# Performance work log

Hardware: AMD Instinct MI355X
Metric: run time of the kernel (lower is better)

## Reference

```python
import jax, jax.numpy as jnp
import numpy as np

V, E, HT, HC = 30000, 300, 256, 256
B, LC, T = 32, 32, 64
NTAG = 9  # output_dim + 2


def lstm_dir(x, lens, Wih, Whh, b, reverse):
    """Variable-length single-direction LSTM (packed-sequence semantics).
    x: [N, T, D], lens: [N] int. Returns outputs [N, T, H] zeroed at pad steps.
    Masked state update keeps h,c frozen at pad steps, so reverse=True starts
    from each sequence's true last element (zeros carry through leading pads).
    """
    N, Tn, _ = x.shape
    H = Whh.shape[1]
    gx = jnp.einsum('ntd,gd->ntg', x, Wih) + b            # [N,T,4H]
    mask = jnp.arange(Tn)[None, :] < lens[:, None]         # [N,T]

    def step(carry, inp):
        h, c = carry
        g_t, m = inp                                       # [N,4H], [N]
        gates = g_t + h @ Whh.T
        i, f, g, o = jnp.split(gates, 4, axis=-1)
        c_new = jax.nn.sigmoid(f) * c + jax.nn.sigmoid(i) * jnp.tanh(g)
        h_new = jax.nn.sigmoid(o) * jnp.tanh(c_new)
        m = m[:, None]
        h2 = jnp.where(m, h_new, h)
        c2 = jnp.where(m, c_new, c)
        return (h2, c2), jnp.where(m, h2, 0.0)

    init = (jnp.zeros((N, H), x.dtype), jnp.zeros((N, H), x.dtype))
    xs = (jnp.swapaxes(gx, 0, 1), mask.T)
    _, ys = jax.lax.scan(step, init, xs, reverse=reverse)
    return jnp.swapaxes(ys, 0, 1)                          # [N,T,H]


def bilstm(x, lens, Wih_f, Whh_f, b_f, Wih_b, Whh_b, b_b):
    hf = lstm_dir(x, lens, Wih_f, Whh_f, b_f, reverse=False)
    hb = lstm_dir(x, lens, Wih_b, Whh_b, b_b, reverse=True)
    return jnp.concatenate([hf, hb], axis=-1)


def setup_inputs() -> dict:
    key = jax.random.key(0)
    ks = jax.random.split(key, 20)
    s = 0.05
    inp = {
        'x': jax.random.randint(ks[0], (B, LC, T), 0, V, dtype=jnp.int32),
        'x_feats': jax.random.normal(ks[1], (B, LC, 64), jnp.float32),
        'x_len': jnp.maximum(jax.random.randint(ks[2], (B,), 0, LC, dtype=jnp.int32), 1),
        'x_chunk_len': jax.random.randint(ks[3], (B, LC), 1, T + 1, dtype=jnp.int32),
        'emb': jax.random.normal(ks[4], (V, E), jnp.float32) * s,
        'tok_Wih_f': jax.random.normal(ks[5], (4 * HT, E), jnp.float32) * s,
        'tok_Whh_f': jax.random.normal(ks[6], (4 * HT, HT), jnp.float32) * s,
        'tok_b_f': jax.random.normal(ks[7], (4 * HT,), jnp.float32) * s,
        'tok_Wih_b': jax.random.normal(ks[8], (4 * HT, E), jnp.float32) * s,
        'tok_Whh_b': jax.random.normal(ks[9], (4 * HT, HT), jnp.float32) * s,
        'tok_b_b': jax.random.normal(ks[10], (4 * HT,), jnp.float32) * s,
        'chk_Wih_f': jax.random.normal(ks[11], (4 * HC, 2 * HT), jnp.float32) * s,
        'chk_Whh_f': jax.random.normal(ks[12], (4 * HC, HC), jnp.float32) * s,
        'chk_b_f': jax.random.normal(ks[13], (4 * HC,), jnp.float32) * s,
        'chk_Wih_b': jax.random.normal(ks[14], (4 * HC, 2 * HT), jnp.float32) * s,
        'chk_Whh_b': jax.random.normal(ks[15], (4 * HC, HC), jnp.float32) * s,
        'chk_b_b': jax.random.normal(ks[16], (4 * HC,), jnp.float32) * s,
        'fc_W': jax.random.normal(ks[17], (NTAG, 2 * HC), jnp.float32) * s,
        'fc_b': jax.random.normal(ks[18], (NTAG,), jnp.float32) * s,
    }
    return inp


def reference(x, x_feats, x_len, x_chunk_len, emb,
              tok_Wih_f, tok_Whh_f, tok_b_f, tok_Wih_b, tok_Whh_b, tok_b_b,
              chk_Wih_f, chk_Whh_f, chk_b_f, chk_Wih_b, chk_Whh_b, chk_b_b,
              fc_W, fc_b):
    b, lc, t = x.shape
    xe = emb[x].reshape(b * lc, t, -1)                     # [B*LC, T, E]
    clens = jnp.clip(x_chunk_len.reshape(-1), 1, t)        # [B*LC]
    h = bilstm(xe, clens, tok_Wih_f, tok_Whh_f, tok_b_f,
               tok_Wih_b, tok_Whh_b, tok_b_b)              # [B*LC, T, 2HT]
    # gather output at last valid timestep (= [fwd final, bwd one-step])
    last = h[jnp.arange(b * lc), clens - 1]                # [B*LC, 2HT]
    chunks = last.reshape(b, lc, -1)                       # [B, LC, 2HT]
    ch = bilstm(chunks, x_len, chk_Wih_f, chk_Whh_f, chk_b_f,
                chk_Wih_b, chk_Whh_b, chk_b_b)             # [B, LC, 2HC]
    # pad_packed(total_length=LC) gives zeros at pad -> fc sees zeros there
    out = ch @ fc_W.T + fc_b                               # [B, LC, NTAG]
    return out
```

## Files before the change

kernel.cpp:

```cpp
#include <hip/hip_runtime.h>


typedef __attribute__((ext_vector_type(8))) short s16x8;
typedef __attribute__((ext_vector_type(4))) float f32x4;
typedef __attribute__((ext_vector_type(2))) unsigned int u32x2;

__device__ __forceinline__ unsigned short f2bf(float f) {
  unsigned u = __builtin_bit_cast(unsigned, f);
  u += 0x7fff + ((u >> 16) & 1);
  return (unsigned short)(u >> 16);
}
__device__ __forceinline__ float bf2f(unsigned short h) {
  unsigned u = ((unsigned)h) << 16;
  return __builtin_bit_cast(float, u);
}
__device__ __forceinline__ float sigm(float x) { return 1.f / (1.f + __expf(-x)); }
__device__ __forceinline__ float tanh_(float x) { return 1.f - 2.f / (__expf(2.f * x) + 1.f); }

union PK8 { s16x8 v; unsigned short u[8]; };

__global__ void prep_weights(const float* __restrict__ wihf, const float* __restrict__ wihb,
                             const float* __restrict__ wcf, const float* __restrict__ wcb,
                             unsigned short* __restrict__ o_wf, unsigned short* __restrict__ o_wb,
                             unsigned short* __restrict__ o_wcf, unsigned short* __restrict__ o_wcb) {
  const int job = blockIdx.y, r = blockIdx.x, tid = threadIdx.x;
  const float* src; unsigned short* dst; int Ks, Kd;
  switch (job) {
    case 0: src = wihf; dst = o_wf;   Ks = 300; Kd = 320; break;
    case 1: src = wihb; dst = o_wb;   Ks = 300; Kd = 320; break;
    case 2: src = wcf;  dst = o_wcf;  Ks = 512; Kd = 512; break;
    default:src = wcb;  dst = o_wcb;  Ks = 512; Kd = 512; break;
  }
  for (int c = tid; c < Kd; c += 256)
    dst[r * Kd + c] = f2bf(c < Ks ? src[r * Ks + c] : 0.f);
}

__global__ __launch_bounds__(256)
void prep_whh_frag(const float* __restrict__ w0, const float* __restrict__ w1,
                   const float* __restrict__ w2,
                   unsigned short* __restrict__ o0, unsigned short* __restrict__ o1,
                   unsigned short* __restrict__ o2) {
  const float* src = blockIdx.y == 0 ? w0 : (blockIdx.y == 1 ? w1 : w2);
  unsigned short* dst = blockIdx.y == 0 ? o0 : (blockIdx.y == 1 ? o1 : o2);
  const int fid = blockIdx.x;
  const int b = fid & 1, g = (fid >> 1) & 3, kt = (fid >> 3) & 7, js = fid >> 6;
  for (int i = threadIdx.x; i < 512; i += 256) {
    const int lane = i >> 3, e = i & 7;
    const int cc = lane & 15, qq = lane >> 4;
    const int row = g * 256 + (js * 2 + b) * 16 + cc;
    const int col = kt * 32 + qq * 8 + e;
    dst[(size_t)fid * 512 + i] = f2bf(src[row * 256 + col]);
  }
}

__global__ void prep_small(const int* __restrict__ x, const int* __restrict__ xcl,
                           int* __restrict__ clens, int* __restrict__ lastv,
                           int* __restrict__ order, int* __restrict__ glen) {
  __shared__ int start[65];
  const int n = threadIdx.x;
  if (n < 65) start[n] = 0;
  __syncthreads();
  int len = xcl[n]; len = len < 1 ? 1 : (len > 64 ? 64 : len);
  clens[n] = len;
  lastv[n] = x[n * 64 + len - 1];
  atomicAdd(&start[len], 1);
  __syncthreads();
  if (n == 0) {
    int acc = 0;
    for (int l = 64; l >= 1; --l) { int h = start[l]; start[l] = acc; acc += h; }
  }
  __syncthreads();
  int pos = atomicAdd(&start[len], 1);
  order[pos] = n;
  __syncthreads();
  if (n < 64) glen[n] = clens[order[n * 16]];
}

__global__ __launch_bounds__(256, 2)
void gemm_bf(const float* __restrict__ A, const int* __restrict__ rowmap,
             int Mrows, int Astride, int Klog, int KP,
             const unsigned short* __restrict__ B, unsigned short* __restrict__ C) {
  __shared__ unsigned short As[128 * 40];
  __shared__ unsigned short Ep[4][64 * 136];
  const int tid = threadIdx.x;
  const int lane = tid & 63, w = tid >> 6;
  const int wrow = w >> 1, wcol = w & 1;
  const int cc = lane & 15, qq = lane >> 4;
  const int m0 = blockIdx.y * 128, n0 = blockIdx.x * 256;

  f32x4 zz = {0.f, 0.f, 0.f, 0.f};
  f32x4 acc[4][8];
#pragma unroll
  for (int i = 0; i < 4; ++i)
#pragma unroll
    for (int j = 0; j < 8; ++j) acc[i][j] = zz;

  const int arow = tid >> 1, ahalf = tid & 1;
  const float* arp = nullptr;
  {
    int av = m0 + arow;
    if (av < Mrows) {
      int amap = rowmap ? rowmap[av] : av;
      arp = A + (long)amap * Astride;
    }
  }

  const int nktiles = KP >> 5;
  for (int kt = 0; kt < nktiles; ++kt) {
    const int k0 = kt << 5;
    __syncthreads();
    {
      const int kb = k0 + ahalf * 16;
      unsigned short hv[16];
      if (arp && kb + 16 <= Klog) {
        const float* p = arp + kb;
#pragma unroll
        for (int i = 0; i < 16; i += 4) {
          f32x4 t = *(const f32x4*)(p + i);
          hv[i] = f2bf(t.x); hv[i + 1] = f2bf(t.y);
          hv[i + 2] = f2bf(t.z); hv[i + 3] = f2bf(t.w);
        }
      } else {
#pragma unroll
        for (int i = 0; i < 16; ++i) {
          float v = (arp && (kb + i) < Klog) ? arp[kb + i] : 0.f;
          hv[i] = f2bf(v);
        }
      }
      PK8 p0, p1;
#pragma unroll
      for (int i = 0; i < 8; ++i) { p0.u[i] = hv[i]; p1.u[i] = hv[8 + i]; }
      *(s16x8*)&As[arow * 40 + ahalf * 16] = p0.v;
      *(s16x8*)&As[arow * 40 + ahalf * 16 + 8] = p1.v;
    }
    __syncthreads();
    s16x8 af[4];
#pragma unroll
    for (int mt = 0; mt < 4; ++mt)
      af[mt] = *(const s16x8*)&As[(wrow * 64 + mt * 16 + cc) * 40 + qq * 8];
#pragma unroll
    for (int nt = 0; nt < 8; ++nt) {
      const unsigned short* bp = B + (long)(n0 + wcol * 128 + nt * 16 + cc) * KP + k0 + qq * 8;
      s16x8 bfr = *(const s16x8*)bp;
#pragma unroll
      for (int mt = 0; mt < 4; ++mt)
        acc[mt][nt] = __builtin_amdgcn_mfma_f32_16x16x32_bf16(af[mt], bfr, acc[mt][nt], 0, 0, 0);
    }
  }
  __syncthreads();
#pragma unroll
  for (int mt = 0; mt < 4; ++mt)
#pragma unroll
    for (int nt = 0; nt < 8; ++nt)
#pragma unroll
      for (int r = 0; r < 4; ++r)
        Ep[w][(mt * 16 + qq * 4 + r) * 136 + nt * 16 + cc] = f2bf(acc[mt][nt][r]);
  __syncthreads();
#pragma unroll
  for (int it = 0; it < 16; ++it) {
    int row = it * 4 + qq;
    s16x8 d = *(const s16x8*)&Ep[w][row * 136 + cc * 8];
    int gm = m0 + wrow * 64 + row;
    int gn = n0 + wcol * 128 + cc * 8;
    if (gm < Mrows) *(s16x8*)&C[(long)gm * 1024 + gn] = d;
  }
}

__global__ void bwd_step(const unsigned short* __restrict__ gxb,
                         const float* __restrict__ bias,
                         float* __restrict__ chunks) {
  const int n = blockIdx.x, j = threadIdx.x;
  const unsigned short* row = gxb + (long)n * 1024;
  float gi = bf2f(row[j]) + bias[j];
  float gg = bf2f(row[512 + j]) + bias[512 + j];
  float go = bf2f(row[768 + j]) + bias[768 + j];
  float cn = sigm(gi) * tanh_(gg);
  chunks[(long)n * 512 + 256 + j] = sigm(go) * tanh_(cn);
}

__global__ __launch_bounds__(256)
void gather_gx(const unsigned short* __restrict__ proj, const int* __restrict__ x,
               const int* __restrict__ order, const int* __restrict__ clens,
               const int* __restrict__ glen, const float* __restrict__ bias,
               unsigned short* __restrict__ gx) {
  const int t = blockIdx.x, p = blockIdx.y, j = threadIdx.x;
  if (t >= glen[p >> 4]) return;
  const int seq = order[p];
  const int len = clens[seq];
  if (t >= len) return;
  unsigned short* dst = gx + (((size_t)(p >> 4) * 64 + t) * 16 + (p & 15)) * 1024 + j * 4;
  const int tok = x[seq * 64 + t];
  const unsigned short* src = proj + (size_t)tok * 1024 + j;
  unsigned v0 = f2bf(bf2f(src[0]) + bias[j]);
  unsigned v1 = f2bf(bf2f(src[256]) + bias[256 + j]);
  unsigned v2 = f2bf(bf2f(src[512]) + bias[512 + j]);
  unsigned v3 = f2bf(bf2f(src[768]) + bias[768 + j]);
  u32x2 pk = {v0 | (v1 << 16), v2 | (v3 << 16)};
  *(u32x2*)dst = pk;
}

__global__ __launch_bounds__(256)
void repack4(const unsigned short* __restrict__ s0, const unsigned short* __restrict__ s1,
             const float* __restrict__ b0, const float* __restrict__ b1,
             unsigned short* __restrict__ d0, unsigned short* __restrict__ d1) {
  const int r = blockIdx.x, j = threadIdx.x;
  const int m = r >> 5, t = r & 31;
  const int mg = m >> 4, m16 = m & 15;
  const unsigned short* s = (blockIdx.y ? s1 : s0) + (size_t)r * 1024;
  const float* bb = blockIdx.y ? b1 : b0;
  unsigned short* d = (blockIdx.y ? d1 : d0) +
                      (size_t)((mg * 32 + t) * 16 + m16) * 1024 + j * 4;
  unsigned v0 = f2bf(bf2f(s[j]) + bb[j]);
  unsigned v1 = f2bf(bf2f(s[256 + j]) + bb[256 + j]);
  unsigned v2 = f2bf(bf2f(s[512 + j]) + bb[512 + j]);
  unsigned v3 = f2bf(bf2f(s[768 + j]) + bb[768 + j]);
  u32x2 pk = {v0 | (v1 << 16), v2 | (v3 << 16)};
  *(u32x2*)d = pk;
}

__global__ __launch_bounds__(1024, 4)
void tok_fwd(const unsigned short* __restrict__ gx,
             const unsigned short* __restrict__ WhP,
             const int* __restrict__ order,
             const int* __restrict__ clens,
             const int* __restrict__ glen,
             float* __restrict__ chunks) {
  extern __shared__ unsigned short smem[];
  unsigned short* hbuf = smem;
  unsigned short* ldsW = smem + 8448;
  int* sg = (int*)(smem + 8448 + 65536);
  int* slen = sg + 16;

  const int tid = threadIdx.x;
  const int lane = tid & 63, w = tid >> 6;
  const int cc = lane & 15, qq = lane >> 4;
  const int gb = blockIdx.x;

  if (tid < 16) {
    int s = order[gb * 16 + tid];
    sg[tid] = s;
    slen[tid] = clens[s];
  }
  for (int i = tid; i < 4224; i += 1024) hbuf[i] = 0;

  const unsigned short* wgl = WhP + ((size_t)(w >> 1) * 64 + (w & 1)) * 512 + lane * 8;
  {
    unsigned short* ld = ldsW + w * 4096 + lane * 8;
#pragma unroll
    for (int kt = 0; kt < 2; ++kt)
#pragma unroll
      for (int g = 0; g < 4; ++g)
        *(s16x8*)&ld[(kt * 4 + g) * 512] = *(const s16x8*)&wgl[(kt * 8 + g * 2) * 512];
  }
  s16x8 Rw[24];
#pragma unroll
  for (int kt = 2; kt < 8; ++kt)
#pragma unroll
    for (int g = 0; g < 4; ++g)
      Rw[(kt - 2) * 4 + g] = *(const s16x8*)&wgl[(kt * 8 + g * 2) * 512];

  __syncthreads();

  const int maxlen = glen[gb];
  const int j = w * 16 + cc;
  int lenr[4];
#pragma unroll
  for (int r = 0; r < 4; ++r) lenr[r] = slen[qq * 4 + r];

  float cst[4];
  unsigned short hreg[4];
#pragma unroll
  for (int r = 0; r < 4; ++r) { cst[r] = 0.f; hreg[r] = 0; }

  const unsigned short* gx0 = gx + (size_t)gb * 64 * 16 * 1024 + j * 4;
  const unsigned short* ldw = ldsW + w * 4096 + lane * 8;
  f32x4 zz = {0.f, 0.f, 0.f, 0.f};

  for (int t = 0; t < maxlen; ++t) {
    const unsigned short* hr = hbuf + (t & 1) * 4224;
    unsigned short* hw = hbuf + ((t & 1) ^ 1) * 4224;

    __syncthreads();

    u32x2 gxp[4];
#pragma unroll
    for (int r = 0; r < 4; ++r)
      gxp[r] = *(const u32x2*)(gx0 + ((size_t)t * 16 + qq * 4 + r) * 1024);

    f32x4 acc[4];
#pragma unroll
    for (int g = 0; g < 4; ++g) acc[g] = zz;

#pragma unroll
    for (int kt = 0; kt < 2; ++kt) {
      s16x8 a0 = *(const s16x8*)&hr[cc * 264 + kt * 32 + qq * 8];
#pragma unroll
      for (int g = 0; g < 4; ++g) {
        s16x8 bf = *(const s16x8*)&ldw[(kt * 4 + g) * 512];
        acc[g] = __builtin_amdgcn_mfma_f32_16x16x32_bf16(a0, bf, acc[g], 0, 0, 0);
      }
    }
#pragma unroll
    for (int kt = 2; kt < 8; ++kt) {
      s16x8 a0 = *(const s16x8*)&hr[cc * 264 + kt * 32 + qq * 8];
#pragma unroll
      for (int g = 0; g < 4; ++g)
        acc[g] = __builtin_amdgcn_mfma_f32_16x16x32_bf16(a0, Rw[(kt - 2) * 4 + g], acc[g], 0, 0, 0);
    }

#pragma unroll
    for (int r = 0; r < 4; ++r) {
      const int m = qq * 4 + r;
      const u32x2 pk = gxp[r];
      float gi = acc[0][r] + bf2f((unsigned short)(pk.x & 0xffff));
      float gf = acc[1][r] + bf2f((unsigned short)(pk.x >> 16));
      float gg = acc[2][r] + bf2f((unsigned short)(pk.y & 0xffff));
      float go = acc[3][r] + bf2f((unsigned short)(pk.y >> 16));
      if (t < lenr[r]) {
        float cn = sigm(gf) * cst[r] + sigm(gi) * tanh_(gg);
        cst[r] = cn;
        hreg[r] = f2bf(sigm(go) * tanh_(cn));
      }
      hw[m * 264 + j] = hreg[r];
    }
  }

#pragma unroll
  for (int r = 0; r < 4; ++r)
    chunks[(size_t)sg[qq * 4 + r] * 512 + j] = bf2f(hreg[r]);
}

__global__ __launch_bounds__(1024, 4)
void chunk_rec(const unsigned short* __restrict__ gxf,
               const unsigned short* __restrict__ gxb,
               const unsigned short* __restrict__ WhPf,
               const unsigned short* __restrict__ WhPb,
               const int* __restrict__ xlen,
               unsigned short* __restrict__ ch) {
  extern __shared__ unsigned short smem[];
  unsigned short* hbuf = smem;
  unsigned short* ldsW = smem + 8448;

  const int tid = threadIdx.x;
  const int lane = tid & 63, w = tid >> 6;
  const int cc = lane & 15, qq = lane >> 4;
  const int dir = blockIdx.x & 1, mg = blockIdx.x >> 1;
  const unsigned short* gx = (dir ? gxb : gxf) + (size_t)mg * 32 * 16 * 1024;
  const unsigned short* WhP = dir ? WhPb : WhPf;

  for (int i = tid; i < 4224; i += 1024) hbuf[i] = 0;

  const unsigned short* wgl = WhP + ((size_t)(w >> 1) * 64 + (w & 1)) * 512 + lane * 8;
  {
    unsigned short* ld = ldsW + w * 4096 + lane * 8;
#pragma unroll
    for (int kt = 0; kt < 2; ++kt)
#pragma unroll
      for (int g = 0; g < 4; ++g)
        *(s16x8*)&ld[(kt * 4 + g) * 512] = *(const s16x8*)&wgl[(kt * 8 + g * 2) * 512];
  }
  s16x8 Rw[24];
#pragma unroll
  for (int kt = 2; kt < 8; ++kt)
#pragma unroll
    for (int g = 0; g < 4; ++g)
      Rw[(kt - 2) * 4 + g] = *(const s16x8*)&wgl[(kt * 8 + g * 2) * 512];

  __syncthreads();

  const int j = w * 16 + cc;
  int lenr[4];
#pragma unroll
  for (int r = 0; r < 4; ++r) {
    int L = xlen[mg * 16 + qq * 4 + r];
    lenr[r] = L > 32 ? 32 : L;
  }

  float cst[4];
  unsigned short hreg[4];
#pragma unroll
  for (int r = 0; r < 4; ++r) { cst[r] = 0.f; hreg[r] = 0; }

  const unsigned short* ldw = ldsW + w * 4096 + lane * 8;
  f32x4 zz = {0.f, 0.f, 0.f, 0.f};

  for (int tt = 0; tt < 32; ++tt) {
    const int t = dir ? (31 - tt) : tt;
    const unsigned short* hr = hbuf + (tt & 1) * 4224;
    unsigned short* hw = hbuf + ((tt & 1) ^ 1) * 4224;

    __syncthreads();

    u32x2 gxp[4];
#pragma unroll
    for (int r = 0; r < 4; ++r)
      gxp[r] = *(const u32x2*)(gx + ((size_t)t * 16 + qq * 4 + r) * 1024 + j * 4);

    f32x4 acc[4];
#pragma unroll
    for (int g = 0; g < 4; ++g) acc[g] = zz;

#pragma unroll
    for (int kt = 0; kt < 2; ++kt) {
      s16x8 a0 = *(const s16x8*)&hr[cc * 264 + kt * 32 + qq * 8];
#pragma unroll
      for (int g = 0; g < 4; ++g) {
        s16x8 bf = *(const s16x8*)&ldw[(kt * 4 + g) * 512];
        acc[g] = __builtin_amdgcn_mfma_f32_16x16x32_bf16(a0, bf, acc[g], 0, 0, 0);
      }
    }
#pragma unroll
    for (int kt = 2; kt < 8; ++kt) {
      s16x8 a0 = *(const s16x8*)&hr[cc * 264 + kt * 32 + qq * 8];
#pragma unroll
      for (int g = 0; g < 4; ++g)
        acc[g] = __builtin_amdgcn_mfma_f32_16x16x32_bf16(a0, Rw[(kt - 2) * 4 + g], acc[g], 0, 0, 0);
    }

#pragma unroll
    for (int r = 0; r < 4; ++r) {
      const int m = qq * 4 + r;
      const u32x2 pk = gxp[r];
      float gi = acc[0][r] + bf2f((unsigned short)(pk.x & 0xffff));
      float gf = acc[1][r] + bf2f((unsigned short)(pk.x >> 16));
      float gg = acc[2][r] + bf2f((unsigned short)(pk.y & 0xffff));
      float go = acc[3][r] + bf2f((unsigned short)(pk.y >> 16));
      unsigned short out16 = 0;
      if (t < lenr[r]) {
        float cn = sigm(gf) * cst[r] + sigm(gi) * tanh_(gg);
        cst[r] = cn;
        hreg[r] = f2bf(sigm(go) * tanh_(cn));
        out16 = hreg[r];
      }
      hw[m * 264 + j] = hreg[r];
      ch[(size_t)((mg * 16 + m) * 32 + t) * 512 + dir * 256 + j] = out16;
    }
  }
}

__global__ __launch_bounds__(64)
void fc_kernel(const unsigned short* __restrict__ ch, const float* __restrict__ W,
               const float* __restrict__ bfc, float* __restrict__ out) {
  const int n = blockIdx.x, lane = threadIdx.x;
  float xv[8];
  const unsigned short* cp = ch + (long)n * 512 + lane * 8;
#pragma unroll
  for (int i = 0; i < 8; ++i) xv[i] = bf2f(cp[i]);
  float s[9];
#pragma unroll
  for (int k = 0; k < 9; ++k) {
    const float* wr = W + k * 512 + lane * 8;
    float t = 0.f;
#pragma unroll
    for (int i = 0; i < 8; ++i) t += xv[i] * wr[i];
    s[k] = t;
  }
#pragma unroll
  for (int off = 32; off; off >>= 1)
#pragma unroll
    for (int k = 0; k < 9; ++k) s[k] += __shfl_down(s[k], off, 64);
  if (lane == 0) {
#pragma unroll
    for (int k = 0; k < 9; ++k) out[n * 9 + k] = s[k] + bfc[k];
  }
}

extern "C" void kernel_launch(void* const* d_in, const int* in_sizes, int n_in,
                              void* d_out, int out_size, void* d_ws, size_t ws_size,
                              hipStream_t stream) {
  const int*   x           = (const int*)d_in[0];
  const int*   x_len       = (const int*)d_in[2];
  const int*   x_chunk_len = (const int*)d_in[3];
  const float* emb         = (const float*)d_in[4];
  const float* tok_Wih_f   = (const float*)d_in[5];
  const float* tok_Whh_f   = (const float*)d_in[6];
  const float* tok_b_f     = (const float*)d_in[7];
  const float* tok_Wih_b   = (const float*)d_in[8];
  const float* tok_b_b     = (const float*)d_in[10];
  const float* chk_Wih_f   = (const float*)d_in[11];
  const float* chk_Whh_f   = (const float*)d_in[12];
  const float* chk_b_f     = (const float*)d_in[13];
  const float* chk_Wih_b   = (const float*)d_in[14];
  const float* chk_Whh_b   = (const float*)d_in[15];
  const float* chk_b_b     = (const float*)d_in[16];
  const float* fc_W        = (const float*)d_in[17];
  const float* fc_b        = (const float*)d_in[18];
  float* out = (float*)d_out;

  char* ws = (char*)d_ws;
  size_t off = 0;
  auto alloc = [&](size_t bytes) -> void* {
    void* p = ws + off;
    off += (bytes + 255) & ~(size_t)255;
    return p;
  };
  unsigned short* Wf   = (unsigned short*)alloc((size_t)1024 * 320 * 2);
  unsigned short* Wb   = (unsigned short*)alloc((size_t)1024 * 320 * 2);
  unsigned short* Wcf  = (unsigned short*)alloc((size_t)1024 * 512 * 2);
  unsigned short* Wcb  = (unsigned short*)alloc((size_t)1024 * 512 * 2);
  unsigned short* WhPtok=(unsigned short*)alloc((size_t)512 * 512 * 2);
  unsigned short* WhPcf= (unsigned short*)alloc((size_t)512 * 512 * 2);
  unsigned short* WhPcb= (unsigned short*)alloc((size_t)512 * 512 * 2);
  unsigned short* proj = (unsigned short*)alloc((size_t)30000 * 1024 * 2);
  unsigned short* gxbb = (unsigned short*)alloc((size_t)1024 * 1024 * 2);
  unsigned short* gxcf = (unsigned short*)alloc((size_t)1024 * 1024 * 2);
  unsigned short* gxcb = (unsigned short*)alloc((size_t)1024 * 1024 * 2);
  unsigned short* gxcfp= (unsigned short*)alloc((size_t)1024 * 1024 * 2);
  unsigned short* gxcbp= (unsigned short*)alloc((size_t)1024 * 1024 * 2);
  float*          chunks = (float*)alloc((size_t)1024 * 512 * 4);
  unsigned short* cho  = (unsigned short*)alloc((size_t)1024 * 512 * 2);
  unsigned short* gxs  = (unsigned short*)alloc((size_t)1024 * 64 * 1024 * 2);
  int* clens = (int*)alloc(1024 * 4);
  int* lastv = (int*)alloc(1024 * 4);
  int* order = (int*)alloc(1024 * 4);
  int* glen  = (int*)alloc(64 * 4);

  hipFuncSetAttribute((const void*)tok_fwd,
                      hipFuncAttributeMaxDynamicSharedMemorySize, 148096);
  hipFuncSetAttribute((const void*)chunk_rec,
                      hipFuncAttributeMaxDynamicSharedMemorySize, 147968);

  prep_weights<<<dim3(1024, 4), 256, 0, stream>>>(
      tok_Wih_f, tok_Wih_b, chk_Wih_f, chk_Wih_b, Wf, Wb, Wcf, Wcb);
  prep_whh_frag<<<dim3(512, 3), 256, 0, stream>>>(
      tok_Whh_f, chk_Whh_f, chk_Whh_b, WhPtok, WhPcf, WhPcb);
  prep_small<<<1, 1024, 0, stream>>>(x, x_chunk_len, clens, lastv, order, glen);

  gemm_bf<<<dim3(4, 235), 256, 0, stream>>>(emb, nullptr, 30000, 300, 300, 320, Wf, proj);
  gemm_bf<<<dim3(4, 8), 256, 0, stream>>>(emb, lastv, 1024, 300, 300, 320, Wb, gxbb);
  bwd_step<<<1024, 256, 0, stream>>>(gxbb, tok_b_b, chunks);
  gather_gx<<<dim3(64, 1024), 256, 0, stream>>>(proj, x, order, clens, glen, tok_b_f, gxs);
  tok_fwd<<<64, 1024, 148096, stream>>>(gxs, WhPtok, order, clens, glen, chunks);
  gemm_bf<<<dim3(4, 8), 256, 0, stream>>>(chunks, nullptr, 1024, 512, 512, 512, Wcf, gxcf);
  gemm_bf<<<dim3(4, 8), 256, 0, stream>>>(chunks, nullptr, 1024, 512, 512, 512, Wcb, gxcb);
  repack4<<<dim3(1024, 2), 256, 0, stream>>>(gxcf, gxcb, chk_b_f, chk_b_b, gxcfp, gxcbp);
  chunk_rec<<<4, 1024, 147968, stream>>>(gxcfp, gxcbp, WhPcf, WhPcb, x_len, cho);
  fc_kernel<<<1024, 64, 0, stream>>>(cho, fc_W, fc_b, out);
}
```

Baseline: 883.6 us.

## Stream recurrent weights from global each step instead of pinning in registers

The recurrent Whh fragments are reordered so each wave's 32 fragments are contiguous. Only the first 8 stay in LDS; the remaining 24 are reloaded from global/L2 every timestep, double-buffered through S/T register sets and overlapped with the MFMAs. This frees the 24 s16x8 registers that used to hold weights, which should lower register pressure and spilling, at the cost of per-step global weight traffic on the serial critical path. The hbuf zeroing now clears both double buffers.

```diff
diff --git a/kernel.cpp b/kernel.cpp
--- a/kernel.cpp
+++ b/kernel.cpp
@@ -4,6 +4,7 @@
 typedef __attribute__((ext_vector_type(8))) short s16x8;
 typedef __attribute__((ext_vector_type(4))) float f32x4;
 typedef __attribute__((ext_vector_type(2))) unsigned int u32x2;
+typedef __attribute__((ext_vector_type(4))) unsigned int u32x4;
 
 __device__ __forceinline__ unsigned short f2bf(float f) {
   unsigned u = __builtin_bit_cast(unsigned, f);
@@ -43,11 +44,11 @@
   const float* src = blockIdx.y == 0 ? w0 : (blockIdx.y == 1 ? w1 : w2);
   unsigned short* dst = blockIdx.y == 0 ? o0 : (blockIdx.y == 1 ? o1 : o2);
   const int fid = blockIdx.x;
-  const int b = fid & 1, g = (fid >> 1) & 3, kt = (fid >> 3) & 7, js = fid >> 6;
+  const int g = fid & 3, kt = (fid >> 2) & 7, jt = fid >> 5;
   for (int i = threadIdx.x; i < 512; i += 256) {
     const int lane = i >> 3, e = i & 7;
     const int cc = lane & 15, qq = lane >> 4;
-    const int row = g * 256 + (js * 2 + b) * 16 + cc;
+    const int row = g * 256 + jt * 16 + cc;
     const int col = kt * 32 + qq * 8 + e;
     dst[(size_t)fid * 512 + i] = f2bf(src[row * 256 + col]);
   }
@@ -241,28 +242,18 @@
     sg[tid] = s;
     slen[tid] = clens[s];
   }
-  for (int i = tid; i < 4224; i += 1024) hbuf[i] = 0;
-
-  const unsigned short* wgl = WhP + ((size_t)(w >> 1) * 64 + (w & 1)) * 512 + lane * 8;
+  for (int i = tid; i < 8448; i += 1024) hbuf[i] = 0;
+
+  const unsigned short* wgl = WhP + ((size_t)w * 8 * 4) * 512 + lane * 8;
   {
     unsigned short* ld = ldsW + w * 4096 + lane * 8;
 #pragma unroll
-    for (int kt = 0; kt < 2; ++kt)
-#pragma unroll
-      for (int g = 0; g < 4; ++g)
-        *(s16x8*)&ld[(kt * 4 + g) * 512] = *(const s16x8*)&wgl[(kt * 8 + g * 2) * 512];
-  }
-  s16x8 Rw[24];
-#pragma unroll
-  for (int kt = 2; kt < 8; ++kt)
-#pragma unroll
-    for (int g = 0; g < 4; ++g)
-      Rw[(kt - 2) * 4 + g] = *(const s16x8*)&wgl[(kt * 8 + g * 2) * 512];
-
+    for (int s = 0; s < 8; ++s)
+      *(s16x8*)&ld[s * 512] = *(const s16x8*)&wgl[s * 512];
+  }
   __syncthreads();
 
   const int maxlen = glen[gb];
-  const int j = w * 16 + cc;
   int lenr[4];
 #pragma unroll
   for (int r = 0; r < 4; ++r) lenr[r] = slen[qq * 4 + r];
@@ -270,8 +261,9 @@
   float cst[4];
   unsigned short hreg[4];
 #pragma unroll
-  for (int r = 0; r < 4; ++r) { cst[r] = 0.f; hreg[r] = 0; }
-
+  for (int i = 0; i < 4; ++i) { cst[i] = 0.f; hreg[i] = 0; }
+
+  const int j = w * 16 + cc;
   const unsigned short* gx0 = gx + (size_t)gb * 64 * 16 * 1024 + j * 4;
   const unsigned short* ldw = ldsW + w * 4096 + lane * 8;
   f32x4 zz = {0.f, 0.f, 0.f, 0.f};
@@ -282,30 +274,77 @@
 
     __syncthreads();
 
+    s16x8 S[4], T[4];
+#pragma unroll
+    for (int g4 = 0; g4 < 4; ++g4)
+      S[g4] = *(const s16x8*)&wgl[(8 + g4) * 512];
     u32x2 gxp[4];
 #pragma unroll
     for (int r = 0; r < 4; ++r)
       gxp[r] = *(const u32x2*)(gx0 + ((size_t)t * 16 + qq * 4 + r) * 1024);
+#pragma unroll
+    for (int g4 = 0; g4 < 4; ++g4)
+      T[g4] = *(const s16x8*)&wgl[(12 + g4) * 512];
 
     f32x4 acc[4];
 #pragma unroll
-    for (int g = 0; g < 4; ++g) acc[g] = zz;
+    for (int g4 = 0; g4 < 4; ++g4) acc[g4] = zz;
 
 #pragma unroll
     for (int kt = 0; kt < 2; ++kt) {
-      s16x8 a0 = *(const s16x8*)&hr[cc * 264 + kt * 32 + qq * 8];
-#pragma unroll
-      for (int g = 0; g < 4; ++g) {
-        s16x8 bf = *(const s16x8*)&ldw[(kt * 4 + g) * 512];
-        acc[g] = __builtin_amdgcn_mfma_f32_16x16x32_bf16(a0, bf, acc[g], 0, 0, 0);
-      }
-    }
-#pragma unroll
-    for (int kt = 2; kt < 8; ++kt) {
-      s16x8 a0 = *(const s16x8*)&hr[cc * 264 + kt * 32 + qq * 8];
-#pragma unroll
-      for (int g = 0; g < 4; ++g)
-        acc[g] = __builtin_amdgcn_mfma_f32_16x16x32_bf16(a0, Rw[(kt - 2) * 4 + g], acc[g], 0, 0, 0);
+      s16x8 a = *(const s16x8*)&hr[cc * 264 + kt * 32 + qq * 8];
+#pragma unroll
+      for (int g4 = 0; g4 < 4; ++g4)
+        acc[g4] = __builtin_amdgcn_mfma_f32_16x16x32_bf16(
+            a, *(const s16x8*)&ldw[(kt * 4 + g4) * 512], acc[g4], 0, 0, 0);
+    }
+    {
+      s16x8 a = *(const s16x8*)&hr[cc * 264 + 2 * 32 + qq * 8];
+#pragma unroll
+      for (int g4 = 0; g4 < 4; ++g4)
+        acc[g4] = __builtin_amdgcn_mfma_f32_16x16x32_bf16(a, S[g4], acc[g4], 0, 0, 0);
+    }
+#pragma unroll
+    for (int g4 = 0; g4 < 4; ++g4)
+      S[g4] = *(const s16x8*)&wgl[(16 + g4) * 512];
+    {
+      s16x8 a = *(const s16x8*)&hr[cc * 264 + 3 * 32 + qq * 8];
+#pragma unroll
+      for (int g4 = 0; g4 < 4; ++g4)
+        acc[g4] = __builtin_amdgcn_mfma_f32_16x16x32_bf16(a, T[g4], acc[g4], 0, 0, 0);
+    }
+#pragma unroll
+    for (int g4 = 0; g4 < 4; ++g4)
+      T[g4] = *(const s16x8*)&wgl[(20 + g4) * 512];
+    {
+      s16x8 a = *(const s16x8*)&hr[cc * 264 + 4 * 32 + qq * 8];
+#pragma unroll
+      for (int g4 = 0; g4 < 4; ++g4)
+        acc[g4] = __builtin_amdgcn_mfma_f32_16x16x32_bf16(a, S[g4], acc[g4], 0, 0, 0);
+    }
+#pragma unroll
+    for (int g4 = 0; g4 < 4; ++g4)
+      S[g4] = *(const s16x8*)&wgl[(24 + g4) * 512];
+    {
+      s16x8 a = *(const s16x8*)&hr[cc * 264 + 5 * 32 + qq * 8];
+#pragma unroll
+      for (int g4 = 0; g4 < 4; ++g4)
+        acc[g4] = __builtin_amdgcn_mfma_f32_16x16x32_bf16(a, T[g4], acc[g4], 0, 0, 0);
+    }
+#pragma unroll
+    for (int g4 = 0; g4 < 4; ++g4)
+      T[g4] = *(const s16x8*)&wgl[(28 + g4) * 512];
+    {
+      s16x8 a = *(const s16x8*)&hr[cc * 264 + 6 * 32 + qq * 8];
+#pragma unroll
+      for (int g4 = 0; g4 < 4; ++g4)
+        acc[g4] = __builtin_amdgcn_mfma_f32_16x16x32_bf16(a, S[g4], acc[g4], 0, 0, 0);
+    }
+    {
+      s16x8 a = *(const s16x8*)&hr[cc * 264 + 7 * 32 + qq * 8];
+#pragma unroll
+      for (int g4 = 0; g4 < 4; ++g4)
+        acc[g4] = __builtin_amdgcn_mfma_f32_16x16x32_bf16(a, T[g4], acc[g4], 0, 0, 0);
     }
 
 #pragma unroll
@@ -348,24 +387,15 @@
   const unsigned short* gx = (dir ? gxb : gxf) + (size_t)mg * 32 * 16 * 1024;
   const unsigned short* WhP = dir ? WhPb : WhPf;
 
-  for (int i = tid; i < 4224; i += 1024) hbuf[i] = 0;
-
-  const unsigned short* wgl = WhP + ((size_t)(w >> 1) * 64 + (w & 1)) * 512 + lane * 8;
+  for (int i = tid; i < 8448; i += 1024) hbuf[i] = 0;
+
+  const unsigned short* wgl = WhP + ((size_t)w * 8 * 4) * 512 + lane * 8;
   {
     unsigned short* ld = ldsW + w * 4096 + lane * 8;
 #pragma unroll
-    for (int kt = 0; kt < 2; ++kt)
-#pragma unroll
-      for (int g = 0; g < 4; ++g)
-        *(s16x8*)&ld[(kt * 4 + g) * 512] = *(const s16x8*)&wgl[(kt * 8 + g * 2) * 512];
-  }
-  s16x8 Rw[24];
-#pragma unroll
-  for (int kt = 2; kt < 8; ++kt)
-#pragma unroll
-    for (int g = 0; g < 4; ++g)
-      Rw[(kt - 2) * 4 + g] = *(const s16x8*)&wgl[(kt * 8 + g * 2) * 512];
-
+    for (int s = 0; s < 8; ++s)
+      *(s16x8*)&ld[s * 512] = *(const s16x8*)&wgl[s * 512];
+  }
   __syncthreads();
 
   const int j = w * 16 + cc;
@@ -379,7 +409,7 @@
   float cst[4];
   unsigned short hreg[4];
 #pragma unroll
-  for (int r = 0; r < 4; ++r) { cst[r] = 0.f; hreg[r] = 0; }
+  for (int i = 0; i < 4; ++i) { cst[i] = 0.f; hreg[i] = 0; }
 
   const unsigned short* ldw = ldsW + w * 4096 + lane * 8;
   f32x4 zz = {0.f, 0.f, 0.f, 0.f};
@@ -391,30 +421,77 @@
 
     __syncthreads();
 
+    s16x8 S[4], T[4];
+#pragma unroll
+    for (int g4 = 0; g4 < 4; ++g4)
+      S[g4] = *(const s16x8*)&wgl[(8 + g4) * 512];
     u32x2 gxp[4];
 #pragma unroll
     for (int r = 0; r < 4; ++r)
       gxp[r] = *(const u32x2*)(gx + ((size_t)t * 16 + qq * 4 + r) * 1024 + j * 4);
+#pragma unroll
+    for (int g4 = 0; g4 < 4; ++g4)
+      T[g4] = *(const s16x8*)&wgl[(12 + g4) * 512];
 
     f32x4 acc[4];
 #pragma unroll
-    for (int g = 0; g < 4; ++g) acc[g] = zz;
+    for (int g4 = 0; g4 < 4; ++g4) acc[g4] = zz;
 
 #pragma unroll
     for (int kt = 0; kt < 2; ++kt) {
-      s16x8 a0 = *(const s16x8*)&hr[cc * 264 + kt * 32 + qq * 8];
-#pragma unroll
-      for (int g = 0; g < 4; ++g) {
-        s16x8 bf = *(const s16x8*)&ldw[(kt * 4 + g) * 512];
-        acc[g] = __builtin_amdgcn_mfma_f32_16x16x32_bf16(a0, bf, acc[g], 0, 0, 0);
-      }
-    }
-#pragma unroll
-    for (int kt = 2; kt < 8; ++kt) {
-      s16x8 a0 = *(const s16x8*)&hr[cc * 264 + kt * 32 + qq * 8];
-#pragma unroll
-      for (int g = 0; g < 4; ++g)
-        acc[g] = __builtin_amdgcn_mfma_f32_16x16x32_bf16(a0, Rw[(kt - 2) * 4 + g], acc[g], 0, 0, 0);
+      s16x8 a = *(const s16x8*)&hr[cc * 264 + kt * 32 + qq * 8];
+#pragma unroll
+      for (int g4 = 0; g4 < 4; ++g4)
+        acc[g4] = __builtin_amdgcn_mfma_f32_16x16x32_bf16(
+            a, *(const s16x8*)&ldw[(kt * 4 + g4) * 512], acc[g4], 0, 0, 0);
+    }
+    {
+      s16x8 a = *(const s16x8*)&hr[cc * 264 + 2 * 32 + qq * 8];
+#pragma unroll
+      for (int g4 = 0; g4 < 4; ++g4)
+        acc[g4] = __builtin_amdgcn_mfma_f32_16x16x32_bf16(a, S[g4], acc[g4], 0, 0, 0);
+    }
+#pragma unroll
+    for (int g4 = 0; g4 < 4; ++g4)
+      S[g4] = *(const s16x8*)&wgl[(16 + g4) * 512];
+    {
+      s16x8 a = *(const s16x8*)&hr[cc * 264 + 3 * 32 + qq * 8];
+#pragma unroll
+      for (int g4 = 0; g4 < 4; ++g4)
+        acc[g4] = __builtin_amdgcn_mfma_f32_16x16x32_bf16(a, T[g4], acc[g4], 0, 0, 0);
+    }
+#pragma unroll
+    for (int g4 = 0; g4 < 4; ++g4)
+      T[g4] = *(const s16x8*)&wgl[(20 + g4) * 512];
+    {
+      s16x8 a = *(const s16x8*)&hr[cc * 264 + 4 * 32 + qq * 8];
+#pragma unroll
+      for (int g4 = 0; g4 < 4; ++g4)
+        acc[g4] = __builtin_amdgcn_mfma_f32_16x16x32_bf16(a, S[g4], acc[g4], 0, 0, 0);
+    }
+#pragma unroll
+    for (int g4 = 0; g4 < 4; ++g4)
+      S[g4] = *(const s16x8*)&wgl[(24 + g4) * 512];
+    {
+      s16x8 a = *(const s16x8*)&hr[cc * 264 + 5 * 32 + qq * 8];
+#pragma unroll
+      for (int g4 = 0; g4 < 4; ++g4)
+        acc[g4] = __builtin_amdgcn_mfma_f32_16x16x32_bf16(a, T[g4], acc[g4], 0, 0, 0);
+    }
+#pragma unroll
+    for (int g4 = 0; g4 < 4; ++g4)
+      T[g4] = *(const s16x8*)&wgl[(28 + g4) * 512];
+    {
+      s16x8 a = *(const s16x8*)&hr[cc * 264 + 6 * 32 + qq * 8];
+#pragma unroll
+      for (int g4 = 0; g4 < 4; ++g4)
+        acc[g4] = __builtin_amdgcn_mfma_f32_16x16x32_bf16(a, S[g4], acc[g4], 0, 0, 0);
+    }
+    {
+      s16x8 a = *(const s16x8*)&hr[cc * 264 + 7 * 32 + qq * 8];
+#pragma unroll
+      for (int g4 = 0; g4 < 4; ++g4)
+        acc[g4] = __builtin_amdgcn_mfma_f32_16x16x32_bf16(a, T[g4], acc[g4], 0, 0, 0);
     }
 
 #pragma unroll
```

Result: slower. 933.4 us (+5.6%).

## Stream recurrent weights per step via double-buffered global-to-LDS loads

Applied to the files above, without the earlier changes.

Both recurrent kernels stop keeping the Whh fragments resident in LDS plus registers. Each timestep they now stream the fragments from global memory into two per-wave LDS stage buffers with global_load_lds, interleaving the loads with the MFMAs using explicit vmcnt and lgkmcnt waits. The weight fragment layout in prep_whh_frag is reordered so each wave reads one contiguous block. This removes about 96 VGPRs of register-held weights, but every step now re-reads the whole weight matrix from L2, which adds memory traffic and wait latency to the serial recurrence.

```diff
diff --git a/kernel.cpp b/kernel.cpp
--- a/kernel.cpp
+++ b/kernel.cpp
@@ -4,6 +4,7 @@
 typedef __attribute__((ext_vector_type(8))) short s16x8;
 typedef __attribute__((ext_vector_type(4))) float f32x4;
 typedef __attribute__((ext_vector_type(2))) unsigned int u32x2;
+typedef __attribute__((ext_vector_type(4))) unsigned int u32x4;
 
 __device__ __forceinline__ unsigned short f2bf(float f) {
   unsigned u = __builtin_bit_cast(unsigned, f);
@@ -16,6 +17,27 @@
 }
 __device__ __forceinline__ float sigm(float x) { return 1.f / (1.f + __expf(-x)); }
 __device__ __forceinline__ float tanh_(float x) { return 1.f - 2.f / (__expf(2.f * x) + 1.f); }
+
+__device__ __forceinline__ void g2l16(const unsigned short* g, unsigned short* l) {
+  __builtin_amdgcn_global_load_lds(
+      (const __attribute__((address_space(1))) void*)g,
+      (__attribute__((address_space(3))) void*)l, 16, 0, 0);
+}
+__device__ __forceinline__ void wait_vm4() {
+  __builtin_amdgcn_sched_barrier(0);
+  asm volatile("s_waitcnt vmcnt(4)" ::: "memory");
+  __builtin_amdgcn_sched_barrier(0);
+}
+__device__ __forceinline__ void wait_vm0() {
+  __builtin_amdgcn_sched_barrier(0);
+  asm volatile("s_waitcnt vmcnt(0)" ::: "memory");
+  __builtin_amdgcn_sched_barrier(0);
+}
+__device__ __forceinline__ void wait_lg0() {
+  __builtin_amdgcn_sched_barrier(0);
+  asm volatile("s_waitcnt lgkmcnt(0)" ::: "memory");
+  __builtin_amdgcn_sched_barrier(0);
+}
 
 union PK8 { s16x8 v; unsigned short u[8]; };
 
@@ -43,11 +65,11 @@
   const float* src = blockIdx.y == 0 ? w0 : (blockIdx.y == 1 ? w1 : w2);
   unsigned short* dst = blockIdx.y == 0 ? o0 : (blockIdx.y == 1 ? o1 : o2);
   const int fid = blockIdx.x;
-  const int b = fid & 1, g = (fid >> 1) & 3, kt = (fid >> 3) & 7, js = fid >> 6;
+  const int g = fid & 3, kt = (fid >> 2) & 7, jt = fid >> 5;
   for (int i = threadIdx.x; i < 512; i += 256) {
     const int lane = i >> 3, e = i & 7;
     const int cc = lane & 15, qq = lane >> 4;
-    const int row = g * 256 + (js * 2 + b) * 16 + cc;
+    const int row = g * 256 + jt * 16 + cc;
     const int col = kt * 32 + qq * 8 + e;
     dst[(size_t)fid * 512 + i] = f2bf(src[row * 256 + col]);
   }
@@ -227,7 +249,8 @@
              float* __restrict__ chunks) {
   extern __shared__ unsigned short smem[];
   unsigned short* hbuf = smem;
-  unsigned short* ldsW = smem + 8448;
+  unsigned short* stage0 = smem + 8448;
+  unsigned short* stage1 = smem + 8448 + 32768;
   int* sg = (int*)(smem + 8448 + 65536);
   int* slen = sg + 16;
 
@@ -241,28 +264,10 @@
     sg[tid] = s;
     slen[tid] = clens[s];
   }
-  for (int i = tid; i < 4224; i += 1024) hbuf[i] = 0;
-
-  const unsigned short* wgl = WhP + ((size_t)(w >> 1) * 64 + (w & 1)) * 512 + lane * 8;
-  {
-    unsigned short* ld = ldsW + w * 4096 + lane * 8;
-#pragma unroll
-    for (int kt = 0; kt < 2; ++kt)
-#pragma unroll
-      for (int g = 0; g < 4; ++g)
-        *(s16x8*)&ld[(kt * 4 + g) * 512] = *(const s16x8*)&wgl[(kt * 8 + g * 2) * 512];
-  }
-  s16x8 Rw[24];
-#pragma unroll
-  for (int kt = 2; kt < 8; ++kt)
-#pragma unroll
-    for (int g = 0; g < 4; ++g)
-      Rw[(kt - 2) * 4 + g] = *(const s16x8*)&wgl[(kt * 8 + g * 2) * 512];
-
+  for (int i = tid; i < 8448; i += 1024) hbuf[i] = 0;
   __syncthreads();
 
   const int maxlen = glen[gb];
-  const int j = w * 16 + cc;
   int lenr[4];
 #pragma unroll
   for (int r = 0; r < 4; ++r) lenr[r] = slen[qq * 4 + r];
@@ -270,11 +275,32 @@
   float cst[4];
   unsigned short hreg[4];
 #pragma unroll
-  for (int r = 0; r < 4; ++r) { cst[r] = 0.f; hreg[r] = 0; }
-
+  for (int i = 0; i < 4; ++i) { cst[i] = 0.f; hreg[i] = 0; }
+
+  const int j = w * 16 + cc;
   const unsigned short* gx0 = gx + (size_t)gb * 64 * 16 * 1024 + j * 4;
-  const unsigned short* ldw = ldsW + w * 4096 + lane * 8;
+  const unsigned short* wglL = WhP + ((size_t)w * 32) * 512 + lane * 8;
+  unsigned short* st0 = stage0 + w * 2048;
+  unsigned short* st1 = stage1 + w * 2048;
+  const unsigned short* sr0 = st0 + lane * 8;
+  const unsigned short* sr1 = st1 + lane * 8;
   f32x4 zz = {0.f, 0.f, 0.f, 0.f};
+
+#define FILLSEC(dst, kt)                                         \
+  do {                                                           \
+    _Pragma("unroll")                                            \
+    for (int g4 = 0; g4 < 4; ++g4)                               \
+      g2l16(wglL + ((kt) * 4 + g4) * 512, (dst) + g4 * 512);     \
+  } while (0)
+
+#define CONSUME(kt, src)                                                     \
+  do {                                                                       \
+    s16x8 a_ = *(const s16x8*)&hr[cc * 264 + (kt) * 32 + qq * 8];            \
+    _Pragma("unroll")                                                        \
+    for (int g4 = 0; g4 < 4; ++g4)                                           \
+      acc[g4] = __builtin_amdgcn_mfma_f32_16x16x32_bf16(                     \
+          a_, *(const s16x8*)&(src)[g4 * 512], acc[g4], 0, 0, 0);            \
+  } while (0)
 
   for (int t = 0; t < maxlen; ++t) {
     const unsigned short* hr = hbuf + (t & 1) * 4224;
@@ -286,27 +312,21 @@
 #pragma unroll
     for (int r = 0; r < 4; ++r)
       gxp[r] = *(const u32x2*)(gx0 + ((size_t)t * 16 + qq * 4 + r) * 1024);
+    FILLSEC(st0, 0);
+    FILLSEC(st1, 1);
 
     f32x4 acc[4];
 #pragma unroll
-    for (int g = 0; g < 4; ++g) acc[g] = zz;
-
-#pragma unroll
-    for (int kt = 0; kt < 2; ++kt) {
-      s16x8 a0 = *(const s16x8*)&hr[cc * 264 + kt * 32 + qq * 8];
-#pragma unroll
-      for (int g = 0; g < 4; ++g) {
-        s16x8 bf = *(const s16x8*)&ldw[(kt * 4 + g) * 512];
-        acc[g] = __builtin_amdgcn_mfma_f32_16x16x32_bf16(a0, bf, acc[g], 0, 0, 0);
-      }
-    }
-#pragma unroll
-    for (int kt = 2; kt < 8; ++kt) {
-      s16x8 a0 = *(const s16x8*)&hr[cc * 264 + kt * 32 + qq * 8];
-#pragma unroll
-      for (int g = 0; g < 4; ++g)
-        acc[g] = __builtin_amdgcn_mfma_f32_16x16x32_bf16(a0, Rw[(kt - 2) * 4 + g], acc[g], 0, 0, 0);
-    }
+    for (int g4 = 0; g4 < 4; ++g4) acc[g4] = zz;
+
+    wait_vm4(); CONSUME(0, sr0); wait_lg0(); FILLSEC(st0, 2);
+    wait_vm4(); CONSUME(1, sr1); wait_lg0(); FILLSEC(st1, 3);
+    wait_vm4(); CONSUME(2, sr0); wait_lg0(); FILLSEC(st0, 4);
+    wait_vm4(); CONSUME(3, sr1); wait_lg0(); FILLSEC(st1, 5);
+    wait_vm4(); CONSUME(4, sr0); wait_lg0(); FILLSEC(st0, 6);
+    wait_vm4(); CONSUME(5, sr1); wait_lg0(); FILLSEC(st1, 7);
+    wait_vm4(); CONSUME(6, sr0);
+    wait_vm0(); CONSUME(7, sr1);
 
 #pragma unroll
     for (int r = 0; r < 4; ++r) {
@@ -324,6 +344,8 @@
       hw[m * 264 + j] = hreg[r];
     }
   }
+#undef FILLSEC
+#undef CONSUME
 
 #pragma unroll
   for (int r = 0; r < 4; ++r)
@@ -339,7 +361,8 @@
                unsigned short* __restrict__ ch) {
   extern __shared__ unsigned short smem[];
   unsigned short* hbuf = smem;
-  unsigned short* ldsW = smem + 8448;
+  unsigned short* stage0 = smem + 8448;
+  unsigned short* stage1 = smem + 8448 + 32768;
 
   const int tid = threadIdx.x;
   const int lane = tid & 63, w = tid >> 6;
@@ -348,24 +371,7 @@
   const unsigned short* gx = (dir ? gxb : gxf) + (size_t)mg * 32 * 16 * 1024;
   const unsigned short* WhP = dir ? WhPb : WhPf;
 
-  for (int i = tid; i < 4224; i += 1024) hbuf[i] = 0;
-
-  const unsigned short* wgl = WhP + ((size_t)(w >> 1) * 64 + (w & 1)) * 512 + lane * 8;
-  {
-    unsigned short* ld = ldsW + w * 4096 + lane * 8;
-#pragma unroll
-    for (int kt = 0; kt < 2; ++kt)
-#pragma unroll
-      for (int g = 0; g < 4; ++g)
-        *(s16x8*)&ld[(kt * 4 + g) * 512] = *(const s16x8*)&wgl[(kt * 8 + g * 2) * 512];
-  }
-  s16x8 Rw[24];
-#pragma unroll
-  for (int kt = 2; kt < 8; ++kt)
-#pragma unroll
-    for (int g = 0; g < 4; ++g)
-      Rw[(kt - 2) * 4 + g] = *(const s16x8*)&wgl[(kt * 8 + g * 2) * 512];
-
+  for (int i = tid; i < 8448; i += 1024) hbuf[i] = 0;
   __syncthreads();
 
   const int j = w * 16 + cc;
@@ -379,10 +385,30 @@
   float cst[4];
   unsigned short hreg[4];
 #pragma unroll
-  for (int r = 0; r < 4; ++r) { cst[r] = 0.f; hreg[r] = 0; }
-
-  const unsigned short* ldw = ldsW + w * 4096 + lane * 8;
+  for (int i = 0; i < 4; ++i) { cst[i] = 0.f; hreg[i] = 0; }
+
+  const unsigned short* wglL = WhP + ((size_t)w * 32) * 512 + lane * 8;
+  unsigned short* st0 = stage0 + w * 2048;
+  unsigned short* st1 = stage1 + w * 2048;
+  const unsigned short* sr0 = st0 + lane * 8;
+  const unsigned short* sr1 = st1 + lane * 8;
   f32x4 zz = {0.f, 0.f, 0.f, 0.f};
+
+#define FILLSEC(dst, kt)                                         \
+  do {                                                           \
+    _Pragma("unroll")                                            \
+    for (int g4 = 0; g4 < 4; ++g4)                               \
+      g2l16(wglL + ((kt) * 4 + g4) * 512, (dst) + g4 * 512);     \
+  } while (0)
+
+#define CONSUME(kt, src)                                                     \
+  do {                                                                       \
+    s16x8 a_ = *(const s16x8*)&hr[cc * 264 + (kt) * 32 + qq * 8];            \
+    _Pragma("unroll")                                                        \
+    for (int g4 = 0; g4 < 4; ++g4)                                           \
+      acc[g4] = __builtin_amdgcn_mfma_f32_16x16x32_bf16(                     \
+          a_, *(const s16x8*)&(src)[g4 * 512], acc[g4], 0, 0, 0);            \
+  } while (0)
 
   for (int tt = 0; tt < 32; ++tt) {
     const int t = dir ? (31 - tt) : tt;
@@ -395,27 +421,21 @@
 #pragma unroll
     for (int r = 0; r < 4; ++r)
       gxp[r] = *(const u32x2*)(gx + ((size_t)t * 16 + qq * 4 + r) * 1024 + j * 4);
+    FILLSEC(st0, 0);
+    FILLSEC(st1, 1);
 
     f32x4 acc[4];
 #pragma unroll
-    for (int g = 0; g < 4; ++g) acc[g] = zz;
-
-#pragma unroll
-    for (int kt = 0; kt < 2; ++kt) {
-      s16x8 a0 = *(const s16x8*)&hr[cc * 264 + kt * 32 + qq * 8];
-#pragma unroll
-      for (int g = 0; g < 4; ++g) {
-        s16x8 bf = *(const s16x8*)&ldw[(kt * 4 + g) * 512];
-        acc[g] = __builtin_amdgcn_mfma_f32_16x16x32_bf16(a0, bf, acc[g], 0, 0, 0);
-      }
-    }
-#pragma unroll
-    for (int kt = 2; kt < 8; ++kt) {
-      s16x8 a0 = *(const s16x8*)&hr[cc * 264 + kt * 32 + qq * 8];
-#pragma unroll
-      for (int g = 0; g < 4; ++g)
-        acc[g] = __builtin_amdgcn_mfma_f32_16x16x32_bf16(a0, Rw[(kt - 2) * 4 + g], acc[g], 0, 0, 0);
-    }
+    for (int g4 = 0; g4 < 4; ++g4) acc[g4] = zz;
+
+    wait_vm4(); CONSUME(0, sr0); wait_lg0(); FILLSEC(st0, 2);
+    wait_vm4(); CONSUME(1, sr1); wait_lg0(); FILLSEC(st1, 3);
+    wait_vm4(); CONSUME(2, sr0); wait_lg0(); FILLSEC(st0, 4);
+    wait_vm4(); CONSUME(3, sr1); wait_lg0(); FILLSEC(st1, 5);
+    wait_vm4(); CONSUME(4, sr0); wait_lg0(); FILLSEC(st0, 6);
+    wait_vm4(); CONSUME(5, sr1); wait_lg0(); FILLSEC(st1, 7);
+    wait_vm4(); CONSUME(6, sr0);
+    wait_vm0(); CONSUME(7, sr1);
 
 #pragma unroll
     for (int r = 0; r < 4; ++r) {
@@ -436,6 +456,8 @@
       ch[(size_t)((mg * 16 + m) * 32 + t) * 512 + dir * 256 + j] = out16;
     }
   }
+#undef FILLSEC
+#undef CONSUME
 }
 
 __global__ __launch_bounds__(64)
```

New measurement: 983.0 us. +11.2%, slower.
